# Optimization experiments

Measured on AMD Instinct MI355X. Metric: run time of the kernel, lower is better.

## Reference

```python
import jax, jax.numpy as jnp
import numpy as np

HD = 128; ED = 64; V = 11; K = 64; L = 1024; LQ = 1024
EPS = 1e-5

def _ln(x, g, b):
    m = jnp.mean(x, axis=-1, keepdims=True)
    v = jnp.mean((x - m) ** 2, axis=-1, keepdims=True)
    return (x - m) / jnp.sqrt(v + EPS) * g + b

def _conv1d(x, w, b):
    # x: [B, C, L], w: [O, I, 3] (torch Conv1d layout), padding=1
    y = jax.lax.conv_general_dilated(x, w, (1,), [(1, 1)],
                                     dimension_numbers=("NCH", "OIH", "NCH"))
    return y + b[None, :, None]

def _enc(ids, emb, c1w, c1b, c2w, c2b, c3w, c3b, n1g, n1b, n2g, n2b, n3g, n3b):
    h = emb[ids].transpose(0, 2, 1)                      # [B, ED, L]
    h = jax.nn.relu(_conv1d(h, c1w, c1b)).transpose(0, 2, 1)
    h = _ln(h, n1g, n1b).transpose(0, 2, 1)
    h = jax.nn.relu(_conv1d(h, c2w, c2b)).transpose(0, 2, 1)
    h = _ln(h, n2g, n2b).transpose(0, 2, 1)
    h = jax.nn.relu(_conv1d(h, c3w, c3b)).transpose(0, 2, 1)
    return _ln(h, n3g, n3b)                              # [B, L, HD]

def setup_inputs() -> dict:
    key = jax.random.key(0)
    ks = iter(jax.random.split(key, 64))
    def nrm(shape, s=0.05):
        return (jax.random.normal(next(ks), shape, dtype=jnp.float32) * s)
    inp = {
        "support_inputs": jax.random.randint(next(ks), (K, L), 0, 10),
        "support_outputs": jax.random.randint(next(ks), (K, L), 0, 10),
        "query_input": jax.random.randint(next(ks), (LQ,), 0, 10),
    }
    for pre in ("qe", "se"):
        inp[pre + "_emb"] = nrm((V, ED)).at[10].set(0.0)
        inp[pre + "_c1w"] = nrm((HD, ED, 3)); inp[pre + "_c1b"] = nrm((HD,))
        inp[pre + "_c2w"] = nrm((HD, HD, 3)); inp[pre + "_c2b"] = nrm((HD,))
        inp[pre + "_c3w"] = nrm((HD, HD, 3)); inp[pre + "_c3b"] = nrm((HD,))
        for i in (1, 2, 3):
            inp[pre + f"_n{i}g"] = jnp.ones((HD,), jnp.float32)
            inp[pre + f"_n{i}b"] = jnp.zeros((HD,), jnp.float32)
    inp["out_emb"] = nrm((V, HD)).at[10].set(0.0)
    inp["dec_w1"] = nrm((HD, 2 * HD)); inp["dec_b1"] = nrm((HD,))
    inp["dec_lng"] = jnp.ones((HD,), jnp.float32)
    inp["dec_lnb"] = jnp.zeros((HD,), jnp.float32)
    inp["dec_w2"] = nrm((10, HD)); inp["dec_b2"] = nrm((10,))
    return inp

def reference(support_inputs, support_outputs, query_input,
              qe_emb, qe_c1w, qe_c1b, qe_c2w, qe_c2b, qe_c3w, qe_c3b,
              qe_n1g, qe_n1b, qe_n2g, qe_n2b, qe_n3g, qe_n3b,
              se_emb, se_c1w, se_c1b, se_c2w, se_c2b, se_c3w, se_c3b,
              se_n1g, se_n1b, se_n2g, se_n2b, se_n3g, se_n3b,
              out_emb, dec_w1, dec_b1, dec_lng, dec_lnb, dec_w2, dec_b2):
    q = _enc(query_input[None], qe_emb, qe_c1w, qe_c1b, qe_c2w, qe_c2b,
             qe_c3w, qe_c3b, qe_n1g, qe_n1b, qe_n2g, qe_n2b, qe_n3g, qe_n3b)[0]   # [LQ, HD]
    s = _enc(support_inputs, se_emb, se_c1w, se_c1b, se_c2w, se_c2b,
             se_c3w, se_c3b, se_n1g, se_n1b, se_n2g, se_n2b, se_n3g, se_n3b)      # [K, L, HD]
    keys = s.reshape(-1, HD)                              # [K*L, HD]
    values = out_emb[support_outputs].reshape(-1, HD)     # [K*L, HD]
    scores = (q @ keys.T) / jnp.sqrt(jnp.float32(HD))     # [LQ, K*L]
    attn = jax.nn.softmax(scores, axis=-1)
    attended = attn @ values                              # [LQ, HD]
    combined = jnp.concatenate([q, attended], axis=-1)    # [LQ, 2*HD]
    h = jax.nn.relu(combined @ dec_w1.T + dec_b1)
    h = _ln(h, dec_lng, dec_lnb)
    return h @ dec_w2.T + dec_b2                          # [LQ, 10]
```

## Files before the change

kernel.cpp:

```cpp
#include <hip/hip_runtime.h>


typedef __attribute__((ext_vector_type(8))) short short8;
typedef __attribute__((ext_vector_type(4))) float f32x4;
typedef __attribute__((ext_vector_type(4))) int int4v;
typedef __attribute__((ext_vector_type(4))) _Float16 half4;

#define EPSV 1e-5f
#define SC 0.12751676f

__device__ __forceinline__ float b2f(unsigned short u) {
  union { unsigned int i; float f; } v; v.i = ((unsigned int)u) << 16; return v.f;
}
__device__ __forceinline__ unsigned short f2b(float f) {
  union { float f; unsigned int i; } v; v.f = f;
  unsigned int r = v.i + 0x7fffu + ((v.i >> 16) & 1u);
  return (unsigned short)(r >> 16);
}
__device__ __forceinline__ f32x4 mfma32(short8 a, short8 b, f32x4 c) {
  return __builtin_amdgcn_mfma_f32_16x16x32_bf16(a, b, c, 0, 0, 0);
}
__device__ __forceinline__ f32x4 mfma16(half4 a, half4 b, f32x4 c) {
  return __builtin_amdgcn_mfma_f32_16x16x16f16(a, b, c, 0, 0, 0);
}
__device__ __forceinline__ void gl_lds16(const void* g, void* l) {
  __builtin_amdgcn_global_load_lds(
      (const __attribute__((address_space(1))) void*)g,
      (__attribute__((address_space(3))) void*)l, 16, 0, 0);
}
__device__ __forceinline__ half4 exp4_pk(f32x4 c) {
  float x0 = exp2f(c[0] * SC - 4.0f), x1 = exp2f(c[1] * SC - 4.0f);
  float x2 = exp2f(c[2] * SC - 4.0f), x3 = exp2f(c[3] * SC - 4.0f);
  union { __fp16 __attribute__((ext_vector_type(2))) h; unsigned int u; } a, b;
  a.h = __builtin_amdgcn_cvt_pkrtz(x0, x1);
  b.h = __builtin_amdgcn_cvt_pkrtz(x2, x3);
  union { unsigned int u[2]; half4 v; } r;
  r.u[0] = a.u; r.u[1] = b.u;
  return r.v;
}

#define OFF_WQ1 0
#define OFF_WQ2 24576
#define OFF_WQ3 73728
#define OFF_WS1 122880
#define OFF_WS2 147456
#define OFF_WS3 196608
#define OFF_EMBQ 245760
#define OFF_EMBS 246464
#define OFF_PBQ 247168
#define OFF_PBS 248320
#define OFF_OEMB 249472
#define OFF_DW1 250880
#define OFF_DB1 283648
#define OFF_DLNG 283776
#define OFF_DLNB 283904
#define OFF_DW2 284032
#define OFF_DB2 285312

__global__ __launch_bounds__(256) void mn_prep(
    const void* qc1w, const void* qc2w, const void* qc3w,
    const void* sc1w, const void* sc2w, const void* sc3w,
    const void* qemb, const void* semb,
    const void* qc1b, const void* qc2b, const void* qc3b,
    const void* qn1g, const void* qn1b, const void* qn2g, const void* qn2b,
    const void* qn3g, const void* qn3b,
    const void* sc1b, const void* sc2b, const void* sc3b,
    const void* sn1g, const void* sn1b, const void* sn2g, const void* sn2b,
    const void* sn3g, const void* sn3b,
    const void* oemb, const void* dw1, const void* db1, const void* dlng,
    const void* dlnb, const void* dw2, const void* db2,
    unsigned short* __restrict__ P, const unsigned int* __restrict__ det) {
  const bool f32m = (*det == 0x3F800000u);
  const int j = blockIdx.y;
  const void* src; int off, n, cin;
  switch (j) {
    case 0:  src = qc1w; off = OFF_WQ1; n = 24576; cin = 64; break;
    case 1:  src = qc2w; off = OFF_WQ2; n = 49152; cin = 128; break;
    case 2:  src = qc3w; off = OFF_WQ3; n = 49152; cin = 128; break;
    case 3:  src = sc1w; off = OFF_WS1; n = 24576; cin = 64; break;
    case 4:  src = sc2w; off = OFF_WS2; n = 49152; cin = 128; break;
    case 5:  src = sc3w; off = OFF_WS3; n = 49152; cin = 128; break;
    case 6:  src = qemb; off = OFF_EMBQ; n = 704; cin = 0; break;
    case 7:  src = semb; off = OFF_EMBS; n = 704; cin = 0; break;
    case 8:  src = qc1b; off = OFF_PBQ + 0; n = 128; cin = 0; break;
    case 9:  src = qc2b; off = OFF_PBQ + 128; n = 128; cin = 0; break;
    case 10: src = qc3b; off = OFF_PBQ + 256; n = 128; cin = 0; break;
    case 11: src = qn1g; off = OFF_PBQ + 384; n = 128; cin = 0; break;
    case 12: src = qn1b; off = OFF_PBQ + 512; n = 128; cin = 0; break;
    case 13: src = qn2g; off = OFF_PBQ + 640; n = 128; cin = 0; break;
    case 14: src = qn2b; off = OFF_PBQ + 768; n = 128; cin = 0; break;
    case 15: src = qn3g; off = OFF_PBQ + 896; n = 128; cin = 0; break;
    case 16: src = qn3b; off = OFF_PBQ + 1024; n = 128; cin = 0; break;
    case 17: src = sc1b; off = OFF_PBS + 0; n = 128; cin = 0; break;
    case 18: src = sc2b; off = OFF_PBS + 128; n = 128; cin = 0; break;
    case 19: src = sc3b; off = OFF_PBS + 256; n = 128; cin = 0; break;
    case 20: src = sn1g; off = OFF_PBS + 384; n = 128; cin = 0; break;
    case 21: src = sn1b; off = OFF_PBS + 512; n = 128; cin = 0; break;
    case 22: src = sn2g; off = OFF_PBS + 640; n = 128; cin = 0; break;
    case 23: src = sn2b; off = OFF_PBS + 768; n = 128; cin = 0; break;
    case 24: src = sn3g; off = OFF_PBS + 896; n = 128; cin = 0; break;
    case 25: src = sn3b; off = OFF_PBS + 1024; n = 128; cin = 0; break;
    case 26: src = oemb; off = OFF_OEMB; n = 1408; cin = 0; break;
    case 27: src = dw1; off = OFF_DW1; n = 32768; cin = 0; break;
    case 28: src = db1; off = OFF_DB1; n = 128; cin = 0; break;
    case 29: src = dlng; off = OFF_DLNG; n = 128; cin = 0; break;
    case 30: src = dlnb; off = OFF_DLNB; n = 128; cin = 0; break;
    case 31: src = dw2; off = OFF_DW2; n = 1280; cin = 0; break;
    default: src = db2; off = OFF_DB2; n = 10; cin = 0; break;
  }
  for (int e = blockIdx.x * 256 + threadIdx.x; e < n; e += gridDim.x * 256) {
    int si = e;
    if (cin) {
      int kw = 3 * cin;
      int o = e / kw, rem = e - o * kw;
      int c = rem >> 3, s = rem & 7;
      int k = ((c ^ (o & 7)) << 3) + s;
      int t = k / cin, i = k - t * cin;
      si = o * kw + i * 3 + t;
    }
    unsigned short v = f32m ? f2b(((const float*)src)[si]) : ((const unsigned short*)src)[si];
    P[off + e] = v;
  }
}

__global__ __launch_bounds__(256) void mn_gtf16(const int* __restrict__ so,
                                                unsigned short* __restrict__ gtf) {
  int t = blockIdx.x * 256 + threadIdx.x;
  int kb = t >> 6, l = t & 63;
  int id = l & 15, g = l >> 4;
  const int* base = so + kb * 16 + g * 4;
  half4 v;
#pragma unroll
  for (int j = 0; j < 4; ++j) {
    int s = base[j];
    bool on = (id < 11) ? (s == id) : (id == 11);
    v[j] = on ? (_Float16)1.0f : (_Float16)0.0f;
  }
  *(half4*)(gtf + (size_t)t * 4) = v;
}

template <int CIN, bool EMBED>
__global__ __launch_bounds__(512, 2) void mn_conv(
    const int* __restrict__ sup_ids, const int* __restrict__ q_ids,
    const unsigned short* __restrict__ in_act,
    const unsigned short* __restrict__ se_emb, const unsigned short* __restrict__ qe_emb,
    const unsigned short* __restrict__ se_wt, const unsigned short* __restrict__ qe_wt,
    const unsigned short* __restrict__ se_b, const unsigned short* __restrict__ qe_b,
    const unsigned short* __restrict__ se_g, const unsigned short* __restrict__ qe_g,
    const unsigned short* __restrict__ se_bt, const unsigned short* __restrict__ qe_bt,
    unsigned short* __restrict__ out_act) {
  constexpr int RB = CIN * 2;
  constexpr int KW = 3 * CIN;
  constexpr int RWB = KW * 2;
  constexpr int WB = 128 * RWB;
  constexpr int XB = 130 * RB;
  constexpr int NK = KW / 32;
  constexpr int WIT = WB / 8192;
  constexpr int CH = RB / 16;
  constexpr int NTASK = 130 * CH;
  constexpr int NT = (NTASK + 511) / 512;
  __shared__ __attribute__((aligned(16))) char lds[WB + XB + 8 * 2176];

  const int b = blockIdx.x;
  int first, nitems;
  if (b < 244)      { first = 2 * b;               nitems = 2; }
  else if (b < 252) { first = 488 + 3 * (b - 244); nitems = 3; }
  else              { first = 512 + 2 * (b - 252); nitems = 2; }
  const bool is_q = (first >= 512);

  const int tid = threadIdx.x;
  const int l = tid & 63, w = tid >> 6;
  const unsigned short* wt = is_q ? qe_wt : se_wt;
  const unsigned short* bs = is_q ? qe_b : se_b;
  const unsigned short* gg = is_q ? qe_g : se_g;
  const unsigned short* bt = is_q ? qe_bt : se_bt;
  const unsigned short* emb = is_q ? qe_emb : se_emb;
  char* xlds = lds + WB;

  {
    const char* wsrc = (const char*)wt + (size_t)(w * WIT) * 1024 + l * 16;
    char* wdst = lds + (w * WIT) * 1024;
#pragma unroll
    for (int i = 0; i < WIT; ++i) gl_lds16(wsrc + i * 1024, wdst + i * 1024);
  }

  int4v vals[NT];
  int dsto[NT];
#define XPHASE1(ITEM)                                                          \
  do {                                                                         \
    int _seq = (ITEM) >> 3, _t0 = ((ITEM) & 7) * 128;                          \
    const int* _ids = EMBED ? (is_q ? q_ids : (sup_ids + _seq * 1024)) : nullptr; \
    const unsigned short* _src = EMBED ? nullptr : in_act + (size_t)_seq * 1024 * CIN; \
    _Pragma("unroll") for (int i = 0; i < NT; ++i) {                           \
      int task = tid + i * 512;                                                \
      int r = task / CH, cb = (task % CH) * 16;                                \
      int p = _t0 + r - 1;                                                     \
      bool ok = (task < NTASK) && p >= 0 && p < 1024;                          \
      int4v v = {0, 0, 0, 0};                                                  \
      if constexpr (EMBED) {                                                   \
        if (ok) v = *(const int4v*)((const char*)emb + _ids[p] * RB + cb);     \
      } else {                                                                 \
        if (ok) v = *(const int4v*)((const char*)_src + (size_t)p * RB + cb);  \
      }                                                                        \
      vals[i] = v;                                                             \
      dsto[i] = (task < NTASK) ? (r * RB + (cb ^ ((r & 7) << 4))) : -1;        \
    }                                                                          \
  } while (0)
#define XPHASE2                                                                \
  do {                                                                         \
    _Pragma("unroll") for (int i = 0; i < NT; ++i)                             \
      if (dsto[i] >= 0) *(int4v*)(xlds + dsto[i]) = vals[i];                   \
  } while (0)

  XPHASE1(first);
  XPHASE2;
  asm volatile("s_waitcnt vmcnt(0)" ::: "memory");
  __syncthreads();

  const int g = l >> 4, q16 = l & 15;
  const int pbase = w * 16;

  float pb[8], pg[8], pt_[8];
#pragma unroll
  for (int ob = 0; ob < 8; ++ob) {
    int o = ob * 16 + q16;
    pb[ob] = b2f(bs[o]); pg[ob] = b2f(gg[o]); pt_[ob] = b2f(bt[o]);
  }
  char* wrep = lds + WB + XB + w * 2176;

  for (int s = 0; s < nitems; ++s) {
    const int item = first + s;
    const int seqI = item >> 3, t0I = (item & 7) * 128;
    const bool more = (s + 1 < nitems);

    if (more) XPHASE1(item + 1);

    f32x4 acc[8];
#pragma unroll
    for (int ob = 0; ob < 8; ++ob) acc[ob] = (f32x4){0.f, 0.f, 0.f, 0.f};

#pragma unroll
    for (int ks = 0; ks < NK; ++ks) {
      const int kk = ks * 32;
      const int t = kk / CIN, i0 = kk % CIN;
      const int cb = (i0 + g * 8) * 2;
      short8 a0;
      {
        int r = pbase + q16 + t;
        a0 = *(const short8*)(xlds + r * RB + (cb ^ ((r & 7) << 4)));
      }
      const int wc = ((ks * 4 + g) ^ (q16 & 7)) << 4;
#pragma unroll
      for (int ob = 0; ob < 8; ++ob) {
        short8 bb = *(const short8*)(lds + (ob * 16 + q16) * RWB + wc);
        acc[ob] = mfma32(a0, bb, acc[ob]);
      }
    }
    __syncthreads();

    if (more) XPHASE2;

    char* obase = (char*)out_act + ((size_t)seqI * 1024 + t0I + pbase) * 256;
#pragma unroll
    for (int h = 0; h < 2; ++h) {
#pragma unroll
      for (int j = 0; j < 2; ++j) {
        const int rg = 2 * h + j;
        float v[8], sm = 0.f, sq = 0.f;
#pragma unroll
        for (int ob = 0; ob < 8; ++ob) {
          float x = acc[ob][rg] + pb[ob];
          x = fmaxf(x, 0.f);
          v[ob] = x; sm += x; sq += x * x;
        }
#pragma unroll
        for (int m = 1; m < 16; m <<= 1) {
          sm += __shfl_xor(sm, m);
          sq += __shfl_xor(sq, m);
        }
        float mean = sm * (1.f / 128.f);
        float var = sq * (1.f / 128.f) - mean * mean;
        float rstd = rsqrtf(var + EPSV);
        unsigned short* dst = (unsigned short*)(wrep + (g * 2 + j) * 272);
#pragma unroll
        for (int ob = 0; ob < 8; ++ob)
          dst[ob * 16 + q16] = f2b((v[ob] - mean) * rstd * pg[ob] + pt_[ob]);
      }
#pragma unroll
      for (int i = 0; i < 2; ++i) {
        int task = i * 64 + l;
        int lr = task >> 4, chk = task & 15;
        int g2 = lr >> 1, jj = lr & 1;
        int p16 = g2 * 4 + 2 * h + jj;
        int4v vv = *(const int4v*)(wrep + lr * 272 + chk * 16);
        *(int4v*)(obase + p16 * 256 + chk * 16) = vv;
      }
    }

    if (more) __syncthreads();
  }
#undef XPHASE1
#undef XPHASE2
}

__global__ __launch_bounds__(256, 2) void mn_attn(const unsigned short* __restrict__ act3,
                                                  const unsigned short* __restrict__ gtf,
                                                  float* __restrict__ Hp) {
  __shared__ __attribute__((aligned(16))) char smem[27648];
  const int tid = threadIdx.x;
  const int l = tid & 63, w = tid >> 6;
  const int g = l >> 4, q16 = l & 15;
  const int ch = blockIdx.x;
  const int qt0 = (blockIdx.y * 4 + w) * 2;

  short8 qfa[4], qfb[4];
  const unsigned short* qrow = act3 + ((size_t)(64 * 1024 + qt0 * 16 + q16)) * 128;
#pragma unroll
  for (int ks = 0; ks < 4; ++ks) {
    qfa[ks] = *(const short8*)(qrow + ks * 32 + g * 8);
    qfb[ks] = *(const short8*)(qrow + 16 * 128 + ks * 32 + g * 8);
  }

  const char* kglob = (const char*)act3 + ((size_t)ch * 1024) * 256;
  const char* gglob = (const char*)gtf + ((size_t)ch * 64) * 512;

  int o0 = (w * 2) * 64 + l, o1 = (w * 2 + 1) * 64 + l;
  int r0s = o0 >> 4, c0s = (o0 & 15) ^ (r0s & 7);
  int r1s = o1 >> 4, c1s = (o1 & 15) ^ (r1s & 7);

#define STAGE(BUF, T)                                                          \
  do {                                                                         \
    const char* _gk = kglob + (size_t)(T) * 8192;                              \
    char* _lk = smem + (BUF) * 8192;                                           \
    gl_lds16(_gk + r0s * 256 + c0s * 16, _lk + (w * 2) * 1024);                \
    gl_lds16(_gk + r1s * 256 + c1s * 16, _lk + (w * 2 + 1) * 1024);            \
    if (w == 0)                                                                \
      gl_lds16(gglob + (size_t)(T) * 1024 + l * 16, smem + 24576 + (BUF) * 1024); \
  } while (0)
#define WAITSTAGE                                                              \
  do {                                                                         \
    if (w == 0) asm volatile("s_waitcnt vmcnt(3)" ::: "memory");               \
    else asm volatile("s_waitcnt vmcnt(2)" ::: "memory");                      \
  } while (0)

  int rc[4], rc1[4];
#pragma unroll
  for (int ks = 0; ks < 4; ++ks) {
    int c = (ks * 4 + g) ^ (q16 & 7);
    rc[ks] = q16 * 256 + c * 16;
    rc1[ks] = (16 + q16) * 256 + c * 16;
  }

  f32x4 hacca = {0.f, 0.f, 0.f, 0.f}, haccb = {0.f, 0.f, 0.f, 0.f};

  STAGE(0, 0);
  STAGE(1, 1);
  WAITSTAGE;
  __builtin_amdgcn_s_barrier();

  for (int it = 0; it < 32; ++it) {
    const int cur = it % 3;
    const char* kb = smem + cur * 8192;
    const char* gb = smem + 24576 + cur * 1024;

    short8 kc0[4], kc1[4];
#pragma unroll
    for (int ks = 0; ks < 4; ++ks) {
      kc0[ks] = *(const short8*)(kb + rc[ks]);
      kc1[ks] = *(const short8*)(kb + rc1[ks]);
    }

    __builtin_amdgcn_s_setprio(1);
    f32x4 c0a = {0.f, 0.f, 0.f, 0.f}, c1a = {0.f, 0.f, 0.f, 0.f};
    f32x4 c0b = {0.f, 0.f, 0.f, 0.f}, c1b = {0.f, 0.f, 0.f, 0.f};
#pragma unroll
    for (int ks = 0; ks < 4; ++ks) {
      c0a = mfma32(kc0[ks], qfa[ks], c0a);
      c1a = mfma32(kc1[ks], qfa[ks], c1a);
      c0b = mfma32(kc0[ks], qfb[ks], c0b);
      c1b = mfma32(kc1[ks], qfb[ks], c1b);
    }

    half4 gf0 = *(const half4*)(gb + l * 8);
    half4 gf1 = *(const half4*)(gb + 512 + l * 8);

    hacca = mfma16(gf0, exp4_pk(c0a), hacca);
    hacca = mfma16(gf1, exp4_pk(c1a), hacca);
    haccb = mfma16(gf0, exp4_pk(c0b), haccb);
    haccb = mfma16(gf1, exp4_pk(c1b), haccb);
    __builtin_amdgcn_s_setprio(0);

    if (it < 30) {
      STAGE((it + 2) % 3, it + 2);
      WAITSTAGE;
    } else {
      asm volatile("s_waitcnt vmcnt(0)" ::: "memory");
    }
    __builtin_amdgcn_s_barrier();
  }
#undef STAGE
#undef WAITSTAGE

  float* outa = Hp + ((size_t)(qt0 * 64 + ch) << 8) + q16;
  float* outb = Hp + ((size_t)((qt0 + 1) * 64 + ch) << 8) + q16;
#pragma unroll
  for (int rg = 0; rg < 4; ++rg) {
    outa[(g * 4 + rg) * 16] = hacca[rg];
    outb[(g * 4 + rg) * 16] = haccb[rg];
  }
}

__global__ __launch_bounds__(256) void mn_combine(const float* __restrict__ Hp,
                                                  const unsigned short* __restrict__ oemb,
                                                  float* __restrict__ att) {
  const int qt = blockIdx.x, tid = threadIdx.x;
  __shared__ float Hs[256];
  float s = 0.f;
  const float* base = Hp + (size_t)qt * 64 * 256 + tid;
  for (int ch = 0; ch < 64; ++ch) s += base[ch * 256];
  Hs[tid] = s;
  __syncthreads();
  for (int e = tid; e < 2048; e += 256) {
    int q = e >> 7, d = e & 127;
    float acc = 0.f;
#pragma unroll
    for (int id = 0; id < 11; ++id) acc += Hs[id * 16 + q] * b2f(oemb[id * 128 + d]);
    att[(size_t)(qt * 16 + q) * 128 + d] = acc / Hs[11 * 16 + q];
  }
}

__global__ __launch_bounds__(128) void mn_dec(
    const unsigned short* __restrict__ act3, const float* __restrict__ att,
    const unsigned short* __restrict__ P, void* __restrict__ out,
    const unsigned int* __restrict__ det) {
  const int row = blockIdx.x, o = threadIdx.x;
  const bool f32m = (*det == 0x3F800000u);
  __shared__ float c[256];
  __shared__ float yv[128];
  __shared__ float red[4];
  c[o] = b2f(act3[((size_t)(64 * 1024) + row) * 128 + o]);
  c[128 + o] = att[(size_t)row * 128 + o];
  __syncthreads();
  float acc = b2f(P[OFF_DB1 + o]);
  const unsigned short* wr = P + OFF_DW1 + o * 256;
  for (int k = 0; k < 256; k += 8) {
    short8 wv = *(const short8*)(wr + k);
#pragma unroll
    for (int j = 0; j < 8; ++j) acc += b2f((unsigned short)wv[j]) * c[k + j];
  }
  float h = fmaxf(acc, 0.f);
  float s = h, sq = h * h;
#pragma unroll
  for (int m = 1; m < 64; m <<= 1) { s += __shfl_xor(s, m); sq += __shfl_xor(sq, m); }
  int wid = o >> 6;
  if ((o & 63) == 0) { red[wid] = s; red[2 + wid] = sq; }
  __syncthreads();
  s = red[0] + red[1]; sq = red[2] + red[3];
  float mean = s * (1.f / 128.f);
  float var = sq * (1.f / 128.f) - mean * mean;
  float rstd = rsqrtf(var + EPSV);
  float y = (h - mean) * rstd * b2f(P[OFF_DLNG + o]) + b2f(P[OFF_DLNB + o]);
  yv[o] = y;
  __syncthreads();
  if (o < 10) {
    float a2 = b2f(P[OFF_DB2 + o]);
    const unsigned short* w2r = P + OFF_DW2 + o * 128;
    for (int k = 0; k < 128; ++k) a2 += b2f(w2r[k]) * yv[k];
    if (f32m) ((float*)out)[(size_t)row * 10 + o] = a2;
    else ((unsigned short*)out)[(size_t)row * 10 + o] = f2b(a2);
  }
}

extern "C" void kernel_launch(void* const* d_in, const int* in_sizes, int n_in,
                              void* d_out, int out_size, void* d_ws, size_t ws_size,
                              hipStream_t stream) {
  (void)in_sizes; (void)n_in; (void)out_size; (void)ws_size;
  const int* sup_in = (const int*)d_in[0];
  const int* sup_out = (const int*)d_in[1];
  const int* q_in = (const int*)d_in[2];

  char* ws = (char*)d_ws;
  unsigned short* P = (unsigned short*)ws;
  unsigned short* actA = (unsigned short*)(ws + 1048576);
  unsigned short* actB = (unsigned short*)(ws + 18087936);
  unsigned short* gtf = (unsigned short*)(ws + 35127296);
  float* Hp = (float*)(ws + 37224448);
  float* attb = (float*)(ws + 41418752);

  const unsigned int* det = (const unsigned int*)d_in[10];

  mn_prep<<<dim3(48, 33), 256, 0, stream>>>(
      d_in[4], d_in[6], d_in[8], d_in[17], d_in[19], d_in[21],
      d_in[3], d_in[16],
      d_in[5], d_in[7], d_in[9],
      d_in[10], d_in[11], d_in[12], d_in[13], d_in[14], d_in[15],
      d_in[18], d_in[20], d_in[22],
      d_in[23], d_in[24], d_in[25], d_in[26], d_in[27], d_in[28],
      d_in[29], d_in[30], d_in[31], d_in[32], d_in[33], d_in[34], d_in[35],
      P, det);
  mn_gtf16<<<1024, 256, 0, stream>>>(sup_out, gtf);
  mn_conv<64, true><<<256, 512, 0, stream>>>(
      sup_in, q_in, nullptr, P + OFF_EMBS, P + OFF_EMBQ, P + OFF_WS1, P + OFF_WQ1,
      P + OFF_PBS + 0, P + OFF_PBQ + 0, P + OFF_PBS + 384, P + OFF_PBQ + 384,
      P + OFF_PBS + 512, P + OFF_PBQ + 512, actA);
  mn_conv<128, false><<<256, 512, 0, stream>>>(
      nullptr, nullptr, actA, nullptr, nullptr, P + OFF_WS2, P + OFF_WQ2,
      P + OFF_PBS + 128, P + OFF_PBQ + 128, P + OFF_PBS + 640, P + OFF_PBQ + 640,
      P + OFF_PBS + 768, P + OFF_PBQ + 768, actB);
  mn_conv<128, false><<<256, 512, 0, stream>>>(
      nullptr, nullptr, actB, nullptr, nullptr, P + OFF_WS3, P + OFF_WQ3,
      P + OFF_PBS + 256, P + OFF_PBQ + 256, P + OFF_PBS + 896, P + OFF_PBQ + 896,
      P + OFF_PBS + 1024, P + OFF_PBQ + 1024, actA);
  mn_attn<<<dim3(64, 8), 256, 0, stream>>>(actA, gtf, Hp);
  mn_combine<<<64, 256, 0, stream>>>(Hp, P + OFF_OEMB, attb);
  mn_dec<<<1024, 128, 0, stream>>>(actA, attb, P, d_out, det);
}
```

Before: 115.1 us.

## Fuse gtf build into prep, fold combine into decoder, double-tile attention pipeline

Folds the one-hot gtf construction into the prep kernel as an extra grid row, and moves the combine step (summing per-chunk partials and projecting through out_emb) into the decoder kernel. Together these drop two kernel launches and the intermediate attended buffer. The attention loop switches from a 3-buffer ring with one barrier per tile to 4 LDS buffers, processing two tiles per phase with one full vmcnt(0) wait and barrier. This halves the barrier count but raises LDS use and removes the partial wait, so loads may overlap less with compute. The decoder now redundantly re-reads the 64 partials for each row rather than once per 16-row tile.

Result: slower. 122.1 us (+6.1%).

```diff
diff --git a/kernel.cpp b/kernel.cpp
--- a/kernel.cpp
+++ b/kernel.cpp
@@ -69,9 +69,26 @@
     const void* sn3g, const void* sn3b,
     const void* oemb, const void* dw1, const void* db1, const void* dlng,
     const void* dlnb, const void* dw2, const void* db2,
-    unsigned short* __restrict__ P, const unsigned int* __restrict__ det) {
+    unsigned short* __restrict__ P, const unsigned int* __restrict__ det,
+    const int* __restrict__ so, unsigned short* __restrict__ gtf) {
+  const int j = blockIdx.y;
+  if (j == 33) {
+    for (int t = blockIdx.x * 256 + threadIdx.x; t < 262144; t += gridDim.x * 256) {
+      int l = t & 63;
+      int id = l & 15, g = l >> 4;
+      const int* base = so + (t >> 6) * 16 + g * 4;
+      half4 v;
+#pragma unroll
+      for (int jj = 0; jj < 4; ++jj) {
+        int s = base[jj];
+        bool on = (id < 11) ? (s == id) : (id == 11);
+        v[jj] = on ? (_Float16)1.0f : (_Float16)0.0f;
+      }
+      *(half4*)(gtf + (size_t)t * 4) = v;
+    }
+    return;
+  }
   const bool f32m = (*det == 0x3F800000u);
-  const int j = blockIdx.y;
   const void* src; int off, n, cin;
   switch (j) {
     case 0:  src = qc1w; off = OFF_WQ1; n = 24576; cin = 64; break;
@@ -123,22 +140,6 @@
   }
 }
 
-__global__ __launch_bounds__(256) void mn_gtf16(const int* __restrict__ so,
-                                                unsigned short* __restrict__ gtf) {
-  int t = blockIdx.x * 256 + threadIdx.x;
-  int kb = t >> 6, l = t & 63;
-  int id = l & 15, g = l >> 4;
-  const int* base = so + kb * 16 + g * 4;
-  half4 v;
-#pragma unroll
-  for (int j = 0; j < 4; ++j) {
-    int s = base[j];
-    bool on = (id < 11) ? (s == id) : (id == 11);
-    v[j] = on ? (_Float16)1.0f : (_Float16)0.0f;
-  }
-  *(half4*)(gtf + (size_t)t * 4) = v;
-}
-
 template <int CIN, bool EMBED>
 __global__ __launch_bounds__(512, 2) void mn_conv(
     const int* __restrict__ sup_ids, const int* __restrict__ q_ids,
@@ -306,7 +307,7 @@
 __global__ __launch_bounds__(256, 2) void mn_attn(const unsigned short* __restrict__ act3,
                                                   const unsigned short* __restrict__ gtf,
                                                   float* __restrict__ Hp) {
-  __shared__ __attribute__((aligned(16))) char smem[27648];
+  __shared__ __attribute__((aligned(16))) char smem[36864];
   const int tid = threadIdx.x;
   const int l = tid & 63, w = tid >> 6;
   const int g = l >> 4, q16 = l & 15;
@@ -335,12 +336,7 @@
     gl_lds16(_gk + r0s * 256 + c0s * 16, _lk + (w * 2) * 1024);                \
     gl_lds16(_gk + r1s * 256 + c1s * 16, _lk + (w * 2 + 1) * 1024);            \
     if (w == 0)                                                                \
-      gl_lds16(gglob + (size_t)(T) * 1024 + l * 16, smem + 24576 + (BUF) * 1024); \
-  } while (0)
-#define WAITSTAGE                                                              \
-  do {                                                                         \
-    if (w == 0) asm volatile("s_waitcnt vmcnt(3)" ::: "memory");               \
-    else asm volatile("s_waitcnt vmcnt(2)" ::: "memory");                      \
+      gl_lds16(gglob + (size_t)(T) * 1024 + l * 16, smem + 32768 + (BUF) * 1024); \
   } while (0)
 
   int rc[4], rc1[4];
@@ -353,53 +349,58 @@
 
   f32x4 hacca = {0.f, 0.f, 0.f, 0.f}, haccb = {0.f, 0.f, 0.f, 0.f};
 
+#define TILE(KB, GB)                                                           \
+  do {                                                                         \
+    short8 kc0[4], kc1[4];                                                     \
+    _Pragma("unroll") for (int ks = 0; ks < 4; ++ks) {                         \
+      kc0[ks] = *(const short8*)((KB) + rc[ks]);                               \
+      kc1[ks] = *(const short8*)((KB) + rc1[ks]);                              \
+    }                                                                          \
+    __builtin_amdgcn_s_setprio(1);                                             \
+    f32x4 c0a = {0.f, 0.f, 0.f, 0.f}, c1a = {0.f, 0.f, 0.f, 0.f};              \
+    f32x4 c0b = {0.f, 0.f, 0.f, 0.f}, c1b = {0.f, 0.f, 0.f, 0.f};              \
+    _Pragma("unroll") for (int ks = 0; ks < 4; ++ks) {                         \
+      c0a = mfma32(kc0[ks], qfa[ks], c0a);                                     \
+      c1a = mfma32(kc1[ks], qfa[ks], c1a);                                     \
+      c0b = mfma32(kc0[ks], qfb[ks], c0b);                                     \
+      c1b = mfma32(kc1[ks], qfb[ks], c1b);                                     \
+    }                                                                          \
+    half4 gf0 = *(const half4*)((GB) + l * 8);                                 \
+    half4 gf1 = *(const half4*)((GB) + 512 + l * 8);                           \
+    hacca = mfma16(gf0, exp4_pk(c0a), hacca);                                  \
+    hacca = mfma16(gf1, exp4_pk(c1a), hacca);                                  \
+    haccb = mfma16(gf0, exp4_pk(c0b), haccb);                                  \
+    haccb = mfma16(gf1, exp4_pk(c1b), haccb);                                  \
+    __builtin_amdgcn_s_setprio(0);                                             \
+  } while (0)
+
   STAGE(0, 0);
   STAGE(1, 1);
-  WAITSTAGE;
+  asm volatile("s_waitcnt vmcnt(0)" ::: "memory");
   __builtin_amdgcn_s_barrier();
 
-  for (int it = 0; it < 32; ++it) {
-    const int cur = it % 3;
-    const char* kb = smem + cur * 8192;
-    const char* gb = smem + 24576 + cur * 1024;
-
-    short8 kc0[4], kc1[4];
-#pragma unroll
-    for (int ks = 0; ks < 4; ++ks) {
-      kc0[ks] = *(const short8*)(kb + rc[ks]);
-      kc1[ks] = *(const short8*)(kb + rc1[ks]);
+  for (int ph = 0; ph < 16; ++ph) {
+    const int ba = (ph & 1) ? 2 : 0;
+    const char* kbA = smem + ba * 8192;
+    const char* gbA = smem + 32768 + ba * 1024;
+    const char* kbB = smem + (ba + 1) * 8192;
+    const char* gbB = smem + 32768 + (ba + 1) * 1024;
+
+    if (ph < 15) {
+      STAGE(ba ^ 2, 2 * ph + 2);
+      STAGE((ba ^ 2) + 1, 2 * ph + 3);
     }
 
-    __builtin_amdgcn_s_setprio(1);
-    f32x4 c0a = {0.f, 0.f, 0.f, 0.f}, c1a = {0.f, 0.f, 0.f, 0.f};
-    f32x4 c0b = {0.f, 0.f, 0.f, 0.f}, c1b = {0.f, 0.f, 0.f, 0.f};
-#pragma unroll
-    for (int ks = 0; ks < 4; ++ks) {
-      c0a = mfma32(kc0[ks], qfa[ks], c0a);
-      c1a = mfma32(kc1[ks], qfa[ks], c1a);
-      c0b = mfma32(kc0[ks], qfb[ks], c0b);
-      c1b = mfma32(kc1[ks], qfb[ks], c1b);
+    TILE(kbA, gbA);
+    TILE(kbB, gbB);
+
+    if (ph < 15) {
+      asm volatile("s_waitcnt vmcnt(0)" ::: "memory");
+      __builtin_amdgcn_s_barrier();
     }
-
-    half4 gf0 = *(const half4*)(gb + l * 8);
-    half4 gf1 = *(const half4*)(gb + 512 + l * 8);
-
-    hacca = mfma16(gf0, exp4_pk(c0a), hacca);
-    hacca = mfma16(gf1, exp4_pk(c1a), hacca);
-    haccb = mfma16(gf0, exp4_pk(c0b), haccb);
-    haccb = mfma16(gf1, exp4_pk(c1b), haccb);
-    __builtin_amdgcn_s_setprio(0);
-
-    if (it < 30) {
-      STAGE((it + 2) % 3, it + 2);
-      WAITSTAGE;
-    } else {
-      asm volatile("s_waitcnt vmcnt(0)" ::: "memory");
-    }
-    __builtin_amdgcn_s_barrier();
   }
 #undef STAGE
-#undef WAITSTAGE
+#undef TILE
 
   float* outa = Hp + ((size_t)(qt0 * 64 + ch) << 8) + q16;
   float* outb = Hp + ((size_t)((qt0 + 1) * 64 + ch) << 8) + q16;
@@ -410,27 +411,8 @@
   }
 }
 
-__global__ __launch_bounds__(256) void mn_combine(const float* __restrict__ Hp,
-                                                  const unsigned short* __restrict__ oemb,
-                                                  float* __restrict__ att) {
-  const int qt = blockIdx.x, tid = threadIdx.x;
-  __shared__ float Hs[256];
-  float s = 0.f;
-  const float* base = Hp + (size_t)qt * 64 * 256 + tid;
-  for (int ch = 0; ch < 64; ++ch) s += base[ch * 256];
-  Hs[tid] = s;
-  __syncthreads();
-  for (int e = tid; e < 2048; e += 256) {
-    int q = e >> 7, d = e & 127;
-    float acc = 0.f;
-#pragma unroll
-    for (int id = 0; id < 11; ++id) acc += Hs[id * 16 + q] * b2f(oemb[id * 128 + d]);
-    att[(size_t)(qt * 16 + q) * 128 + d] = acc / Hs[11 * 16 + q];
-  }
-}
-
 __global__ __launch_bounds__(128) void mn_dec(
-    const unsigned short* __restrict__ act3, const float* __restrict__ att,
+    const unsigned short* __restrict__ act3, const float* __restrict__ Hp,
     const unsigned short* __restrict__ P, void* __restrict__ out,
     const unsigned int* __restrict__ det) {
   const int row = blockIdx.x, o = threadIdx.x;
@@ -438,8 +420,26 @@
   __shared__ float c[256];
   __shared__ float yv[128];
   __shared__ float red[4];
+  __shared__ float hsum[12];
+
+  const float* hbase = Hp + ((size_t)(row >> 4) * 64 << 8) + (row & 15);
+  if (o < 96) {
+    int id = o >> 3, part = o & 7;
+    float s = 0.f;
+#pragma unroll
+    for (int cc = 0; cc < 8; ++cc) s += hbase[(part * 8 + cc) * 256 + id * 16];
+#pragma unroll
+    for (int m = 1; m < 8; m <<= 1) s += __shfl_xor(s, m);
+    if (part == 0) hsum[id] = s;
+  }
   c[o] = b2f(act3[((size_t)(64 * 1024) + row) * 128 + o]);
-  c[128 + o] = att[(size_t)row * 128 + o];
+  __syncthreads();
+  {
+    float a = 0.f;
+#pragma unroll
+    for (int id = 0; id < 11; ++id) a += hsum[id] * b2f(P[OFF_OEMB + id * 128 + o]);
+    c[128 + o] = a / hsum[11];
+  }
   __syncthreads();
   float acc = b2f(P[OFF_DB1 + o]);
   const unsigned short* wr = P + OFF_DW1 + o * 256;
@@ -485,11 +485,10 @@
   unsigned short* actB = (unsigned short*)(ws + 18087936);
   unsigned short* gtf = (unsigned short*)(ws + 35127296);
   float* Hp = (float*)(ws + 37224448);
-  float* attb = (float*)(ws + 41418752);
 
   const unsigned int* det = (const unsigned int*)d_in[10];
 
-  mn_prep<<<dim3(48, 33), 256, 0, stream>>>(
+  mn_prep<<<dim3(48, 34), 256, 0, stream>>>(
       d_in[4], d_in[6], d_in[8], d_in[17], d_in[19], d_in[21],
       d_in[3], d_in[16],
       d_in[5], d_in[7], d_in[9],
@@ -497,8 +496,7 @@
       d_in[18], d_in[20], d_in[22],
       d_in[23], d_in[24], d_in[25], d_in[26], d_in[27], d_in[28],
       d_in[29], d_in[30], d_in[31], d_in[32], d_in[33], d_in[34], d_in[35],
-      P, det);
-  mn_gtf16<<<1024, 256, 0, stream>>>(sup_out, gtf);
+      P, det, sup_out, gtf);
   mn_conv<64, true><<<256, 512, 0, stream>>>(
       sup_in, q_in, nullptr, P + OFF_EMBS, P + OFF_EMBQ, P + OFF_WS1, P + OFF_WQ1,
       P + OFF_PBS + 0, P + OFF_PBQ + 0, P + OFF_PBS + 384, P + OFF_PBQ + 384,
@@ -512,6 +510,5 @@
       P + OFF_PBS + 256, P + OFF_PBQ + 256, P + OFF_PBS + 896, P + OFF_PBQ + 896,
       P + OFF_PBS + 1024, P + OFF_PBQ + 1024, actA);
   mn_attn<<<dim3(64, 8), 256, 0, stream>>>(actA, gtf, Hp);
-  mn_combine<<<64, 256, 0, stream>>>(Hp, P + OFF_OEMB, attb);
-  mn_dec<<<1024, 128, 0, stream>>>(actA, attb, P, d_out, det);
-}
+  mn_dec<<<1024, 128, 0, stream>>>(actA, Hp, P, d_out, det);
+}
```

## Retile conv waves to 32 positions by 64 channels with cross-wave LayerNorm

Applied to the files above, without the earlier changes.

Each wave now computes a 32-position by 64-output-channel tile instead of 16 positions by 128 channels. The A fragment is reused across two position tiles and each weight fragment is shared by two MFMAs, which cuts LDS weight reads per MFMA. Because LayerNorm spans all 128 channels, partial sums and sums of squares now go through an LDS scratch buffer and need an extra block barrier. The output staging buffer shrinks to match.

New measurement: 120.1 us. +4.3%, slower.

```diff
diff --git a/kernel.cpp b/kernel.cpp
--- a/kernel.cpp
+++ b/kernel.cpp
@@ -159,7 +159,7 @@
   constexpr int CH = RB / 16;
   constexpr int NTASK = 130 * CH;
   constexpr int NT = (NTASK + 511) / 512;
-  __shared__ __attribute__((aligned(16))) char lds[WB + XB + 8 * 2176];
+  __shared__ __attribute__((aligned(16))) char lds[WB + XB + 2048 + 8 * 1152];
 
   const int b = blockIdx.x;
   int first, nitems;
@@ -176,6 +176,8 @@
   const unsigned short* bt = is_q ? qe_bt : se_bt;
   const unsigned short* emb = is_q ? qe_emb : se_emb;
   char* xlds = lds + WB;
+  float* part = (float*)(lds + WB + XB);
+  char* wrep = lds + WB + XB + 2048 + w * 1152;
 
   {
     const char* wsrc = (const char*)wt + (size_t)(w * WIT) * 1024 + l * 16;
@@ -218,15 +220,15 @@
   __syncthreads();
 
   const int g = l >> 4, q16 = l & 15;
-  const int pbase = w * 16;
-
-  float pb[8], pg[8], pt_[8];
-#pragma unroll
-  for (int ob = 0; ob < 8; ++ob) {
-    int o = ob * 16 + q16;
+  const int pr = w & 3, oc = w >> 2;
+  const int pbase = pr * 32;
+
+  float pb[4], pg[4], pt_[4];
+#pragma unroll
+  for (int ob = 0; ob < 4; ++ob) {
+    int o = oc * 64 + ob * 16 + q16;
     pb[ob] = b2f(bs[o]); pg[ob] = b2f(gg[o]); pt_[ob] = b2f(bt[o]);
   }
-  char* wrep = lds + WB + XB + w * 2176;
 
   for (int s = 0; s < nitems; ++s) {
     const int item = first + s;
@@ -235,65 +237,87 @@
 
     if (more) XPHASE1(item + 1);
 
-    f32x4 acc[8];
-#pragma unroll
-    for (int ob = 0; ob < 8; ++ob) acc[ob] = (f32x4){0.f, 0.f, 0.f, 0.f};
+    f32x4 acc[2][4];
+#pragma unroll
+    for (int pt = 0; pt < 2; ++pt)
+#pragma unroll
+      for (int ob = 0; ob < 4; ++ob) acc[pt][ob] = (f32x4){0.f, 0.f, 0.f, 0.f};
 
 #pragma unroll
     for (int ks = 0; ks < NK; ++ks) {
       const int kk = ks * 32;
       const int t = kk / CIN, i0 = kk % CIN;
       const int cb = (i0 + g * 8) * 2;
-      short8 a0;
+      short8 a0, a1;
       {
         int r = pbase + q16 + t;
         a0 = *(const short8*)(xlds + r * RB + (cb ^ ((r & 7) << 4)));
+        r += 16;
+        a1 = *(const short8*)(xlds + r * RB + (cb ^ ((r & 7) << 4)));
       }
       const int wc = ((ks * 4 + g) ^ (q16 & 7)) << 4;
 #pragma unroll
-      for (int ob = 0; ob < 8; ++ob) {
-        short8 bb = *(const short8*)(lds + (ob * 16 + q16) * RWB + wc);
-        acc[ob] = mfma32(a0, bb, acc[ob]);
+      for (int ob = 0; ob < 4; ++ob) {
+        short8 bb = *(const short8*)(lds + (oc * 64 + ob * 16 + q16) * RWB + wc);
+        acc[0][ob] = mfma32(a0, bb, acc[0][ob]);
+        acc[1][ob] = mfma32(a1, bb, acc[1][ob]);
       }
     }
     __syncthreads();
 
     if (more) XPHASE2;
 
-    char* obase = (char*)out_act + ((size_t)seqI * 1024 + t0I + pbase) * 256;
-#pragma unroll
-    for (int h = 0; h < 2; ++h) {
-#pragma unroll
-      for (int j = 0; j < 2; ++j) {
-        const int rg = 2 * h + j;
-        float v[8], sm = 0.f, sq = 0.f;
-#pragma unroll
-        for (int ob = 0; ob < 8; ++ob) {
-          float x = acc[ob][rg] + pb[ob];
-          x = fmaxf(x, 0.f);
-          v[ob] = x; sm += x; sq += x * x;
+#pragma unroll
+    for (int pt = 0; pt < 2; ++pt)
+#pragma unroll
+      for (int rg = 0; rg < 4; ++rg) {
+        float sm = 0.f, sq = 0.f;
+#pragma unroll
+        for (int ob = 0; ob < 4; ++ob) {
+          float x = fmaxf(acc[pt][ob][rg] + pb[ob], 0.f);
+          sm += x; sq += x * x;
         }
 #pragma unroll
         for (int m = 1; m < 16; m <<= 1) {
           sm += __shfl_xor(sm, m);
           sq += __shfl_xor(sq, m);
         }
-        float mean = sm * (1.f / 128.f);
-        float var = sq * (1.f / 128.f) - mean * mean;
-        float rstd = rsqrtf(var + EPSV);
-        unsigned short* dst = (unsigned short*)(wrep + (g * 2 + j) * 272);
-#pragma unroll
-        for (int ob = 0; ob < 8; ++ob)
-          dst[ob * 16 + q16] = f2b((v[ob] - mean) * rstd * pg[ob] + pt_[ob]);
+        if (q16 == 0) {
+          int pos = pbase + pt * 16 + g * 4 + rg;
+          part[pos * 4 + oc * 2] = sm;
+          part[pos * 4 + oc * 2 + 1] = sq;
+        }
       }
-#pragma unroll
-      for (int i = 0; i < 2; ++i) {
-        int task = i * 64 + l;
-        int lr = task >> 4, chk = task & 15;
-        int g2 = lr >> 1, jj = lr & 1;
-        int p16 = g2 * 4 + 2 * h + jj;
-        int4v vv = *(const int4v*)(wrep + lr * 272 + chk * 16);
-        *(int4v*)(obase + p16 * 256 + chk * 16) = vv;
+    __syncthreads();
+
+    char* obase = (char*)out_act + ((size_t)seqI * 1024 + t0I + pbase) * 256 + oc * 128;
+#pragma unroll
+    for (int pt = 0; pt < 2; ++pt) {
+#pragma unroll
+      for (int h = 0; h < 2; ++h) {
+#pragma unroll
+        for (int j = 0; j < 2; ++j) {
+          const int rg = 2 * h + j;
+          const int pos = pbase + pt * 16 + g * 4 + rg;
+          float sm = part[pos * 4] + part[pos * 4 + 2];
+          float sq = part[pos * 4 + 1] + part[pos * 4 + 3];
+          float mean = sm * (1.f / 128.f);
+          float var = sq * (1.f / 128.f) - mean * mean;
+          float rstd = rsqrtf(var + EPSV);
+          unsigned short* dst = (unsigned short*)(wrep + (g * 2 + j) * 144);
+#pragma unroll
+          for (int ob = 0; ob < 4; ++ob) {
+            float x = fmaxf(acc[pt][ob][rg] + pb[ob], 0.f);
+            dst[ob * 16 + q16] = f2b((x - mean) * rstd * pg[ob] + pt_[ob]);
+          }
+        }
+        {
+          int lr = l >> 3, chk = l & 7;
+          int g2 = lr >> 1, jj = lr & 1;
+          int posw = pt * 16 + g2 * 4 + 2 * h + jj;
+          int4v vv = *(const int4v*)(wrep + lr * 144 + chk * 16);
+          *(int4v*)(obase + posw * 256 + chk * 16) = vv;
+        }
       }
     }
 
```
